# Performance work log

Hardware: AMD Instinct MI355X
Metric: run time of the kernel (lower is better)

The kernel has to match this reference:

```python
import jax, jax.numpy as jnp
import numpy as np

B, S1, S2, H, H2, D, K = 1, 1024, 8192, 32, 8, 128, 128


def setup_inputs() -> dict:
    key = jax.random.key(0)
    k1, k2, k3, k4 = jax.random.split(key, 4)
    q = jax.random.normal(k1, (B, S1, H, D), dtype=jnp.float16)
    k = jax.random.normal(k2, (B, S2, H2, D), dtype=jnp.float16)
    v = jax.random.normal(k3, (B, S2, H2, D), dtype=jnp.float16)
    sparse_indices = jax.random.randint(k4, (B, S1, H2, K), 0, S2, dtype=jnp.int32)
    return {"q": q, "k": k, "v": v, "sparse_indices": sparse_indices}


def reference(q, k, v, sparse_indices):
    # q: [B,S1,H,D]  k,v: [B,S2,H2,D]  sparse_indices: [B,S1,H2,K]
    b, s1, h, d = q.shape
    h2 = sparse_indices.shape[2]
    g = h // h2  # GQA group size
    scale = 1.0 / np.sqrt(d).astype(np.float32)
    qg = q.reshape(b, s1, h2, g, d)  # group queries per kv head
    b_idx = jnp.arange(b)[:, None, None, None]
    h_idx = jnp.arange(h2)[None, None, :, None]
    # gather per-query sparse KV sets: [B,S1,H2,K,D]
    kg = k[b_idx, sparse_indices, h_idx]
    vg = v[b_idx, sparse_indices, h_idx]
    scores = jnp.einsum('bshgd,bshkd->bshgk', qg, kg).astype(jnp.float32) * scale
    p = jax.nn.softmax(scores, axis=-1).astype(q.dtype)
    out = jnp.einsum('bshgk,bshkd->bshgd', p, vg)  # [B,S1,H2,G,D]
    return out.reshape(b, s1, h, d).astype(jnp.float16)
```

## Files before the change

### kernel.cpp

```cpp
#include <hip/hip_runtime.h>
#include <stdint.h>
#include <math.h>

#define NH 32
#define NH2 8
#define DD 128
#define KSEL 128
#define GG 4
#define S2MASK 8191

typedef _Float16 h8   __attribute__((ext_vector_type(8)));
typedef __fp16   hp2  __attribute__((ext_vector_type(2)));
typedef float    f32x4 __attribute__((ext_vector_type(4)));

static __device__ __forceinline__ h8 cvt8(float4 a, float4 b) {
  union { h8 v; hp2 p[4]; } u;
  u.p[0] = __builtin_amdgcn_cvt_pkrtz(a.x, a.y);
  u.p[1] = __builtin_amdgcn_cvt_pkrtz(a.z, a.w);
  u.p[2] = __builtin_amdgcn_cvt_pkrtz(b.x, b.y);
  u.p[3] = __builtin_amdgcn_cvt_pkrtz(b.z, b.w);
  return u.v;
}

__global__ __launch_bounds__(256) void sparse_attn_kernel(
    const float* __restrict__ q, const float* __restrict__ k,
    const float* __restrict__ v, const int* __restrict__ idx,
    float* __restrict__ out) {
  __shared__ int sIdx[4][KSEL];
  __shared__ __align__(16) float sP[4][KSEL][GG];

  const int tid = threadIdx.x;
  const int w = tid >> 6;
  const int lane = tid & 63;
  const int h2 = blockIdx.x & 7;
  const int s1 = ((blockIdx.x >> 3) << 2) + w;

  const int* ip = idx + (s1 * NH2 + h2) * KSEL;
  sIdx[w][lane]      = ip[lane] & S2MASK;
  sIdx[w][lane + 64] = ip[lane + 64] & S2MASK;

  const int m  = lane & 15;
  const int kg = lane >> 4;

  h8 aq[4];
#pragma unroll
  for (int t = 0; t < 4; ++t)
#pragma unroll
    for (int i = 0; i < 8; ++i) aq[t][i] = (_Float16)0;
  if (m < GG) {
    const float* qp = q + (s1 * NH + h2 * GG + m) * DD + kg * 8;
#pragma unroll
    for (int t = 0; t < 4; ++t) {
      float4 f0 = *(const float4*)(qp + 32 * t);
      float4 f1 = *(const float4*)(qp + 32 * t + 4);
      aq[t] = cvt8(f0, f1);
    }
  }

  __syncthreads();

  const float scale = 0.08838834764831845f;

#pragma unroll 2
  for (int nt = 0; nt < 8; ++nt) {
    const int s2 = sIdx[w][nt * 16 + m];
    const float* kp = k + (s2 * NH2 + h2) * DD + kg * 8;
    f32x4 acc = {0.f, 0.f, 0.f, 0.f};
#pragma unroll
    for (int t = 0; t < 4; ++t) {
      float4 f0 = *(const float4*)(kp + 32 * t);
      float4 f1 = *(const float4*)(kp + 32 * t + 4);
      acc = __builtin_amdgcn_mfma_f32_16x16x32_f16(aq[t], cvt8(f0, f1), acc, 0, 0, 0);
    }
    if (lane < 16) {
      float4 sc = make_float4(acc[0] * scale, acc[1] * scale,
                              acc[2] * scale, acc[3] * scale);
      *(float4*)&sP[w][nt * 16 + lane][0] = sc;
    }
  }
  __syncthreads();

  {
    float4 p0 = *(const float4*)&sP[w][lane][0];
    float4 p1 = *(const float4*)&sP[w][lane + 64][0];
    float4 mx = make_float4(fmaxf(p0.x, p1.x), fmaxf(p0.y, p1.y),
                            fmaxf(p0.z, p1.z), fmaxf(p0.w, p1.w));
#pragma unroll
    for (int off = 1; off < 64; off <<= 1) {
      mx.x = fmaxf(mx.x, __shfl_xor(mx.x, off));
      mx.y = fmaxf(mx.y, __shfl_xor(mx.y, off));
      mx.z = fmaxf(mx.z, __shfl_xor(mx.z, off));
      mx.w = fmaxf(mx.w, __shfl_xor(mx.w, off));
    }
    float4 e0 = make_float4(__expf(p0.x - mx.x), __expf(p0.y - mx.y),
                            __expf(p0.z - mx.z), __expf(p0.w - mx.w));
    float4 e1 = make_float4(__expf(p1.x - mx.x), __expf(p1.y - mx.y),
                            __expf(p1.z - mx.z), __expf(p1.w - mx.w));
    float4 sm = make_float4(e0.x + e1.x, e0.y + e1.y, e0.z + e1.z, e0.w + e1.w);
#pragma unroll
    for (int off = 1; off < 64; off <<= 1) {
      sm.x += __shfl_xor(sm.x, off);
      sm.y += __shfl_xor(sm.y, off);
      sm.z += __shfl_xor(sm.z, off);
      sm.w += __shfl_xor(sm.w, off);
    }
    float4 inv = make_float4(1.f / fmaxf(sm.x, 1e-30f), 1.f / fmaxf(sm.y, 1e-30f),
                             1.f / fmaxf(sm.z, 1e-30f), 1.f / fmaxf(sm.w, 1e-30f));
    *(float4*)&sP[w][lane][0] =
        make_float4(e0.x * inv.x, e0.y * inv.y, e0.z * inv.z, e0.w * inv.w);
    *(float4*)&sP[w][lane + 64][0] =
        make_float4(e1.x * inv.x, e1.y * inv.y, e1.z * inv.z, e1.w * inv.w);
  }
  __syncthreads();

  float a00 = 0.f, a01 = 0.f, a10 = 0.f, a11 = 0.f;
  float a20 = 0.f, a21 = 0.f, a30 = 0.f, a31 = 0.f;
  const float* vb = v + h2 * DD + lane * 2;
#pragma unroll 8
  for (int j = 0; j < KSEL; ++j) {
    const int s2 = sIdx[w][j];
    const float2 vv = *(const float2*)(vb + (size_t)s2 * (NH2 * DD));
    const float4 p = *(const float4*)&sP[w][j][0];
    a00 = fmaf(p.x, vv.x, a00); a01 = fmaf(p.x, vv.y, a01);
    a10 = fmaf(p.y, vv.x, a10); a11 = fmaf(p.y, vv.y, a11);
    a20 = fmaf(p.z, vv.x, a20); a21 = fmaf(p.z, vv.y, a21);
    a30 = fmaf(p.w, vv.x, a30); a31 = fmaf(p.w, vv.y, a31);
  }

  float* op = out + (s1 * NH + h2 * GG) * DD + lane * 2;
  *(float2*)(op + 0 * DD) = make_float2(a00, a01);
  *(float2*)(op + 1 * DD) = make_float2(a10, a11);
  *(float2*)(op + 2 * DD) = make_float2(a20, a21);
  *(float2*)(op + 3 * DD) = make_float2(a30, a31);
}

extern "C" void kernel_launch(void* const* d_in, const int* in_sizes, int n_in,
                              void* d_out, int out_size, void* d_ws, size_t ws_size,
                              hipStream_t stream) {
  const float* q = (const float*)d_in[0];
  const float* k = (const float*)d_in[1];
  const float* v = (const float*)d_in[2];
  const int* idx = (const int*)d_in[3];
  float* out = (float*)d_out;
  sparse_attn_kernel<<<dim3(2048), dim3(256), 0, stream>>>(q, k, v, idx, out);
}
```

Baseline: 194.2 us.

## Pre-convert K/V to fp16 in workspace before sparse attention gather

Adds a pre-pass kernel that converts the whole K and V tensors from fp32 to fp16 in the workspace, then runs a new attention kernel that gathers the half-precision rows. The gathers then move half as many bytes, the in-loop conversion for K is dropped, and row offsets are precomputed in shared memory. In exchange, every call streams all of K and V (about 8M elements each) through the conversion, even though only the indexed rows are needed. Whether that dense pass is cheaper than the savings on the random gathers is unclear. If the workspace is too small, it falls back to the old fp32 kernel.

```diff
diff --git a/kernel.cpp b/kernel.cpp
--- a/kernel.cpp
+++ b/kernel.cpp
@@ -8,8 +8,10 @@
 #define KSEL 128
 #define GG 4
 #define S2MASK 8191
+#define KVELTS (8192 * NH2 * DD)
 
 typedef _Float16 h8   __attribute__((ext_vector_type(8)));
+typedef _Float16 h2t  __attribute__((ext_vector_type(2)));
 typedef __fp16   hp2  __attribute__((ext_vector_type(2)));
 typedef float    f32x4 __attribute__((ext_vector_type(4)));
 
@@ -22,7 +24,135 @@
   return u.v;
 }
 
-__global__ __launch_bounds__(256) void sparse_attn_kernel(
+__global__ __launch_bounds__(256) void convert_kv(
+    const float4* __restrict__ kf, const float4* __restrict__ vf,
+    ushort4* __restrict__ kh, ushort4* __restrict__ vh, int n4) {
+  int i = blockIdx.x * blockDim.x + threadIdx.x;
+  const int stride = gridDim.x * blockDim.x;
+  union { ushort4 u; hp2 p[2]; } ua;
+  for (; i < n4; i += stride) {
+    float4 a = kf[i];
+    ua.p[0] = __builtin_amdgcn_cvt_pkrtz(a.x, a.y);
+    ua.p[1] = __builtin_amdgcn_cvt_pkrtz(a.z, a.w);
+    kh[i] = ua.u;
+    float4 b = vf[i];
+    ua.p[0] = __builtin_amdgcn_cvt_pkrtz(b.x, b.y);
+    ua.p[1] = __builtin_amdgcn_cvt_pkrtz(b.z, b.w);
+    vh[i] = ua.u;
+  }
+}
+
+__global__ __launch_bounds__(256) void sparse_attn_f16(
+    const float* __restrict__ q, const _Float16* __restrict__ kh,
+    const _Float16* __restrict__ vh, const int* __restrict__ idx,
+    float* __restrict__ out) {
+  __shared__ int sOff[4][KSEL];
+  __shared__ __align__(16) float sP[4][KSEL][GG];
+
+  const int tid = threadIdx.x;
+  const int w = tid >> 6;
+  const int lane = tid & 63;
+  const int h2 = blockIdx.x & 7;
+  const int s1 = ((blockIdx.x >> 3) << 2) + w;
+
+  const int* ip = idx + (s1 * NH2 + h2) * KSEL;
+  sOff[w][lane]      = (ip[lane]      & S2MASK) * (NH2 * DD);
+  sOff[w][lane + 64] = (ip[lane + 64] & S2MASK) * (NH2 * DD);
+
+  const int m  = lane & 15;
+  const int kg = lane >> 4;
+
+  h8 aq[4];
+#pragma unroll
+  for (int t = 0; t < 4; ++t)
+#pragma unroll
+    for (int i = 0; i < 8; ++i) aq[t][i] = (_Float16)0;
+  if (m < GG) {
+    const float* qp = q + (s1 * NH + h2 * GG + m) * DD + kg * 8;
+#pragma unroll
+    for (int t = 0; t < 4; ++t) {
+      float4 f0 = *(const float4*)(qp + 32 * t);
+      float4 f1 = *(const float4*)(qp + 32 * t + 4);
+      aq[t] = cvt8(f0, f1);
+    }
+  }
+
+  __syncthreads();
+
+  const float scale = 0.08838834764831845f;
+
+#pragma unroll 2
+  for (int nt = 0; nt < 8; ++nt) {
+    const _Float16* kp = kh + sOff[w][nt * 16 + m] + h2 * DD + kg * 8;
+    f32x4 acc = {0.f, 0.f, 0.f, 0.f};
+#pragma unroll
+    for (int t = 0; t < 4; ++t) {
+      h8 bk = *(const h8*)(kp + 32 * t);
+      acc = __builtin_amdgcn_mfma_f32_16x16x32_f16(aq[t], bk, acc, 0, 0, 0);
+    }
+    if (lane < 16) {
+      float4 sc = make_float4(acc[0] * scale, acc[1] * scale,
+                              acc[2] * scale, acc[3] * scale);
+      *(float4*)&sP[w][nt * 16 + lane][0] = sc;
+    }
+  }
+  __syncthreads();
+
+  {
+    float4 p0 = *(const float4*)&sP[w][lane][0];
+    float4 p1 = *(const float4*)&sP[w][lane + 64][0];
+    float4 mx = make_float4(fmaxf(p0.x, p1.x), fmaxf(p0.y, p1.y),
+                            fmaxf(p0.z, p1.z), fmaxf(p0.w, p1.w));
+#pragma unroll
+    for (int off = 1; off < 64; off <<= 1) {
+      mx.x = fmaxf(mx.x, __shfl_xor(mx.x, off));
+      mx.y = fmaxf(mx.y, __shfl_xor(mx.y, off));
+      mx.z = fmaxf(mx.z, __shfl_xor(mx.z, off));
+      mx.w = fmaxf(mx.w, __shfl_xor(mx.w, off));
+    }
+    float4 e0 = make_float4(__expf(p0.x - mx.x), __expf(p0.y - mx.y),
+                            __expf(p0.z - mx.z), __expf(p0.w - mx.w));
+    float4 e1 = make_float4(__expf(p1.x - mx.x), __expf(p1.y - mx.y),
+                            __expf(p1.z - mx.z), __expf(p1.w - mx.w));
+    float4 sm = make_float4(e0.x + e1.x, e0.y + e1.y, e0.z + e1.z, e0.w + e1.w);
+#pragma unroll
+    for (int off = 1; off < 64; off <<= 1) {
+      sm.x += __shfl_xor(sm.x, off);
+      sm.y += __shfl_xor(sm.y, off);
+      sm.z += __shfl_xor(sm.z, off);
+      sm.w += __shfl_xor(sm.w, off);
+    }
+    float4 inv = make_float4(1.f / fmaxf(sm.x, 1e-30f), 1.f / fmaxf(sm.y, 1e-30f),
+                             1.f / fmaxf(sm.z, 1e-30f), 1.f / fmaxf(sm.w, 1e-30f));
+    *(float4*)&sP[w][lane][0] =
+        make_float4(e0.x * inv.x, e0.y * inv.y, e0.z * inv.z, e0.w * inv.w);
+    *(float4*)&sP[w][lane + 64][0] =
+        make_float4(e1.x * inv.x, e1.y * inv.y, e1.z * inv.z, e1.w * inv.w);
+  }
+  __syncthreads();
+
+  float a00 = 0.f, a01 = 0.f, a10 = 0.f, a11 = 0.f;
+  float a20 = 0.f, a21 = 0.f, a30 = 0.f, a31 = 0.f;
+  const _Float16* vb = vh + h2 * DD + lane * 2;
+#pragma unroll 8
+  for (int j = 0; j < KSEL; ++j) {
+    const h2t vv = *(const h2t*)(vb + sOff[w][j]);
+    const float vx = (float)vv[0], vy = (float)vv[1];
+    const float4 p = *(const float4*)&sP[w][j][0];
+    a00 = fmaf(p.x, vx, a00); a01 = fmaf(p.x, vy, a01);
+    a10 = fmaf(p.y, vx, a10); a11 = fmaf(p.y, vy, a11);
+    a20 = fmaf(p.z, vx, a20); a21 = fmaf(p.z, vy, a21);
+    a30 = fmaf(p.w, vx, a30); a31 = fmaf(p.w, vy, a31);
+  }
+
+  float* op = out + (s1 * NH + h2 * GG) * DD + lane * 2;
+  *(float2*)(op + 0 * DD) = make_float2(a00, a01);
+  *(float2*)(op + 1 * DD) = make_float2(a10, a11);
+  *(float2*)(op + 2 * DD) = make_float2(a20, a21);
+  *(float2*)(op + 3 * DD) = make_float2(a30, a31);
+}
+
+__global__ __launch_bounds__(256) void sparse_attn_f32(
     const float* __restrict__ q, const float* __restrict__ k,
     const float* __restrict__ v, const int* __restrict__ idx,
     float* __restrict__ out) {
@@ -56,11 +186,9 @@
       aq[t] = cvt8(f0, f1);
     }
   }
-
   __syncthreads();
 
   const float scale = 0.08838834764831845f;
-
 #pragma unroll 2
   for (int nt = 0; nt < 8; ++nt) {
     const int s2 = sIdx[w][nt * 16 + m];
@@ -142,5 +270,16 @@
   const float* v = (const float*)d_in[2];
   const int* idx = (const int*)d_in[3];
   float* out = (float*)d_out;
-  sparse_attn_kernel<<<dim3(2048), dim3(256), 0, stream>>>(q, k, v, idx, out);
-}
+
+  const size_t need = (size_t)2 * KVELTS * sizeof(_Float16);
+  if (ws_size >= need) {
+    _Float16* kh = (_Float16*)d_ws;
+    _Float16* vh = kh + KVELTS;
+    convert_kv<<<dim3(2048), dim3(256), 0, stream>>>(
+        (const float4*)k, (const float4*)v,
+        (ushort4*)kh, (ushort4*)vh, KVELTS / 4);
+    sparse_attn_f16<<<dim3(2048), dim3(256), 0, stream>>>(q, kh, vh, idx, out);
+  } else {
+    sparse_attn_f32<<<dim3(2048), dim3(256), 0, stream>>>(q, k, v, idx, out);
+  }
+}
```

Measured after the change: 173.1 us. 10.9% less time.
